# Optimization experiments

Measured on AMD Instinct MI355X. Metric: run time of the kernel, lower is better.

## Reference

```python
import jax, jax.numpy as jnp
import numpy as np

B, T, D, H, K, M = 2, 2048, 1024, 16, 3, 16384
HD = D // H
SCALE = D * (H ** 0.5)  # faithful to source: n_embd / n_head**(-0.5)


def _normalize(v, axis=-1, eps=1e-12):
    # torch F.normalize: v / max(||v||, eps)
    n = jnp.sqrt(jnp.sum(v * v, axis=axis, keepdims=True))
    return v / jnp.maximum(n, eps)


def setup_inputs() -> dict:
    key = jax.random.key(0)
    ks = jax.random.split(key, 12)
    s = 1.0 / np.sqrt(D)
    return {
        "x": jax.random.normal(ks[0], (B, T, D), jnp.float32),
        "Wq": jax.random.normal(ks[1], (D, D), jnp.float32) * s,
        "bq": jax.random.normal(ks[2], (D,), jnp.float32) * 0.01,
        "Wk": jax.random.normal(ks[3], (D, D), jnp.float32) * s,
        "bk": jax.random.normal(ks[4], (D,), jnp.float32) * 0.01,
        "Wv": jax.random.normal(ks[5], (D, D), jnp.float32) * s,
        "bv": jax.random.normal(ks[6], (D,), jnp.float32) * 0.01,
        "Wo": jax.random.normal(ks[7], (D, D), jnp.float32) * s,
        "bo": jax.random.normal(ks[8], (D,), jnp.float32) * 0.01,
        "gate_bias": jax.random.normal(ks[9], (H, 1, 1), jnp.float32),
        "mem_bank": jax.random.normal(ks[10], (B, M, 2, D), jnp.float32) * s,
        "knn_idx": jax.random.randint(ks[11], (B, T, K), 0, M, jnp.int32),
    }


def reference(x, Wq, bq, Wk, bk, Wv, bv, Wo, bo, gate_bias, mem_bank, knn_idx):
    b, t, d = x.shape
    # projections + L2-normalize q,k (as in source)
    q = _normalize(x @ Wq.T + bq)
    k = _normalize(x @ Wk.T + bk)
    v = x @ Wv.T + bv
    # split heads: b t (h hd) -> b h t hd
    q = q.reshape(b, t, H, HD).transpose(0, 2, 1, 3)
    k = k.reshape(b, t, H, HD).transpose(0, 2, 1, 3)
    v = v.reshape(b, t, H, HD).transpose(0, 2, 1, 3)
    # local causal attention (hand-rolled, dropout is eval no-op)
    qk = jnp.einsum('bhid,bhjd->bhij', q, k) * SCALE  # [b,h,t,t]
    causal = jnp.triu(jnp.ones((t, t), dtype=bool), 1)
    qk = jnp.where(causal, -jnp.inf, qk)
    attn = jax.nn.softmax(qk, axis=-1)
    qkv = jnp.einsum('bhij,bhjd->bhid', attn, v)  # [b,h,t,hd]
    # kNN memory retrieval: gather top-k (key,value) memories per token
    mem = mem_bank[jnp.arange(b)[:, None, None], knn_idx]  # [b,t,k,2,D]
    mem_k = mem[..., 0, :].reshape(b, t, K, H, HD).transpose(0, 3, 1, 2, 4)  # [b,h,t,k,hd]
    mem_v = mem[..., 1, :].reshape(b, t, K, H, HD).transpose(0, 3, 1, 2, 4)
    mem_qk = jnp.einsum('bhtd,bhtkd->bhtk', q.astype(jnp.float32), mem_k) * SCALE
    mem_attn = jax.nn.softmax(mem_qk, axis=-1)
    mem_qkv = jnp.einsum('bhtk,bhtkd->bhtd', mem_attn, mem_v)
    # per-head gated blend, bf16 round-trip (source casts to bfloat16)
    combined = mem_qkv * gate_bias + qkv * (1.0 - gate_bias)  # gate [H,1,1] broadcasts
    combined = combined.astype(jnp.bfloat16).astype(jnp.float32)
    y = combined.transpose(0, 2, 1, 3).reshape(b, t, d)  # b h t hd -> b t D
    return y @ Wo.T + bo
```

## Files before the change

kernel.cpp:

```cpp
#include <hip/hip_runtime.h>
#include <math.h>

#define B_ 2
#define T_ 2048
#define D_ 1024
#define H_ 16
#define HD_ 64
#define M_ 16384
#define SCALE_F 4096.0f
#define LDP 3072
#define ST 72

using short8 = __attribute__((ext_vector_type(8))) short;
using bf16x8 = __attribute__((ext_vector_type(8))) __bf16;
using f32x4  = __attribute__((ext_vector_type(4))) float;

__device__ __forceinline__ unsigned short f2bf(float x){
  unsigned u = __builtin_bit_cast(unsigned, x);
  u += 0x7fffu + ((u >> 16) & 1u);
  return (unsigned short)(u >> 16);
}
__device__ __forceinline__ float bf2f(unsigned short h){
  unsigned u = ((unsigned)h) << 16;
  return __builtin_bit_cast(float, u);
}

__device__ __forceinline__ float wsum(float v){
  #pragma unroll
  for (int off = 32; off; off >>= 1) v += __shfl_xor(v, off);
  return v;
}

__device__ __forceinline__ void ld_g2l16(const unsigned short* g, unsigned short* l){
  __builtin_amdgcn_global_load_lds(
      (const __attribute__((address_space(1))) void*)g,
      (__attribute__((address_space(3))) void*)l, 16, 0, 0);
}

__global__ __launch_bounds__(256)
void cvt_all(const float* __restrict__ x, const float* __restrict__ Wq,
             const float* __restrict__ Wk, const float* __restrict__ Wv,
             const float* __restrict__ Wo,
             unsigned short* __restrict__ Xhi, unsigned short* __restrict__ Xlo,
             unsigned short* __restrict__ Whi, unsigned short* __restrict__ Wlo,
             unsigned short* __restrict__ Wohi)
{
  const int i = blockIdx.x*256 + threadIdx.x;
  const float* src; unsigned short* hi; unsigned short* lo = nullptr; int rel;
  if      (i < 1048576){ src = x;  hi = Xhi;            lo = Xlo;            rel = i; }
  else if (i < 1310720){ src = Wq; hi = Whi;            lo = Wlo;            rel = i - 1048576; }
  else if (i < 1572864){ src = Wk; hi = Whi + 1048576;  lo = Wlo + 1048576;  rel = i - 1310720; }
  else if (i < 1835008){ src = Wv; hi = Whi + 2097152;                       rel = i - 1572864; }
  else                 { src = Wo; hi = Wohi;                                rel = i - 1835008; }
  float4 v = *(const float4*)(src + (size_t)rel*4);
  unsigned short h0=f2bf(v.x), h1=f2bf(v.y), h2=f2bf(v.z), h3=f2bf(v.w);
  uint2 hh; hh.x = (unsigned)h0 | ((unsigned)h1 << 16);
            hh.y = (unsigned)h2 | ((unsigned)h3 << 16);
  *(uint2*)(hi + (size_t)rel*4) = hh;
  if (lo){
    uint2 ll;
    ll.x = (unsigned)f2bf(v.x-bf2f(h0)) | ((unsigned)f2bf(v.y-bf2f(h1)) << 16);
    ll.y = (unsigned)f2bf(v.z-bf2f(h2)) | ((unsigned)f2bf(v.w-bf2f(h3)) << 16);
    *(uint2*)(lo + (size_t)rel*4) = ll;
  }
}

template<bool COMP>
__global__ __launch_bounds__(256)
void gemm_lds(const unsigned short* __restrict__ Ahi_g, const unsigned short* __restrict__ Alo_g,
              const unsigned short* __restrict__ Bhi_g, const unsigned short* __restrict__ Blo_g,
              const float* __restrict__ bias0, const float* __restrict__ bias1,
              const float* __restrict__ bias2,
              float* __restrict__ C, int ldc)
{
  __shared__ __align__(16) unsigned short Ah[128*32];
  __shared__ __align__(16) unsigned short Bh[128*32];
  __shared__ __align__(16) unsigned short Al[COMP ? 128*32 : 8];
  __shared__ __align__(16) unsigned short Bl[COMP ? 128*32 : 8];

  const int tid = threadIdx.x, lane = tid & 63, wv = tid >> 6;
  const int wm = wv >> 1, wn = wv & 1;
  const int mi = lane & 15, quad = lane >> 4;
  const int n0 = blockIdx.x * 128;
  const int m0 = blockIdx.y * 128;
  const int seg = n0 >> 10;
  const float* bias = (seg == 0) ? bias0 : (seg == 1) ? bias1 : bias2;
  const int nw = n0 & 1023;
  const bool comp = COMP && (seg < 2);

  f32x4 acc[4][4];
  #pragma unroll
  for (int a = 0; a < 4; ++a)
    #pragma unroll
    for (int b = 0; b < 4; ++b)
      acc[a][b] = (f32x4){0.f, 0.f, 0.f, 0.f};

  for (int k0 = 0; k0 < 1024; k0 += 32){
    __syncthreads();
    #pragma unroll
    for (int t = 0; t < 2; ++t){
      int j = wv*128 + t*64 + lane;
      int row = j >> 2, c16 = j & 3;
      size_t ga = (size_t)(m0 + row)*1024 + k0 + c16*8;
      size_t gb = (size_t)(n0 + row)*1024 + k0 + c16*8;
      ld_g2l16(Ahi_g + ga, Ah + j*8);
      ld_g2l16(Bhi_g + gb, Bh + j*8);
      if (comp){
        ld_g2l16(Alo_g + ga, Al + j*8);
        ld_g2l16(Blo_g + gb, Bl + j*8);
      }
    }
    __syncthreads();

    bf16x8 ah[4], al[4];
    #pragma unroll
    for (int a = 0; a < 4; ++a){
      int r = wm*64 + a*16 + mi;
      ah[a] = __builtin_bit_cast(bf16x8, *(const short8*)(Ah + r*32 + quad*8));
      if (comp)
        al[a] = __builtin_bit_cast(bf16x8, *(const short8*)(Al + r*32 + quad*8));
    }
    #pragma unroll
    for (int b = 0; b < 4; ++b){
      int r = wn*64 + b*16 + mi;
      bf16x8 bh = __builtin_bit_cast(bf16x8, *(const short8*)(Bh + r*32 + quad*8));
      if (comp){
        bf16x8 bl = __builtin_bit_cast(bf16x8, *(const short8*)(Bl + r*32 + quad*8));
        #pragma unroll
        for (int a = 0; a < 4; ++a){
          acc[a][b] = __builtin_amdgcn_mfma_f32_16x16x32_bf16(al[a], bh, acc[a][b], 0, 0, 0);
          acc[a][b] = __builtin_amdgcn_mfma_f32_16x16x32_bf16(ah[a], bl, acc[a][b], 0, 0, 0);
          acc[a][b] = __builtin_amdgcn_mfma_f32_16x16x32_bf16(ah[a], bh, acc[a][b], 0, 0, 0);
        }
      } else {
        #pragma unroll
        for (int a = 0; a < 4; ++a)
          acc[a][b] = __builtin_amdgcn_mfma_f32_16x16x32_bf16(ah[a], bh, acc[a][b], 0, 0, 0);
      }
    }
  }
  #pragma unroll
  for (int a = 0; a < 4; ++a)
    #pragma unroll
    for (int b = 0; b < 4; ++b)
      #pragma unroll
      for (int r = 0; r < 4; ++r){
        int row  = m0 + wm*64 + a*16 + quad*4 + r;
        int coll = wn*64 + b*16 + mi;
        C[(size_t)row*ldc + n0 + coll] = acc[a][b][r] + bias[nw + coll];
      }
}

__global__ __launch_bounds__(256)
void norm_split(const float* __restrict__ P,
                unsigned short* __restrict__ Qhi, unsigned short* __restrict__ Qlo,
                unsigned short* __restrict__ Khi, unsigned short* __restrict__ Klo,
                unsigned short* __restrict__ Vbf)
{
  const int row = blockIdx.x, tid = threadIdx.x;
  const int bb = row >> 11, t = row & 2047;
  const int lane = tid & 63, wv = tid >> 6;
  const size_t base = (size_t)row * LDP;
  float4 q4 = *(const float4*)(P + base + tid*4);
  float4 k4 = *(const float4*)(P + base + 1024 + tid*4);
  float4 v4 = *(const float4*)(P + base + 2048 + tid*4);
  float sq = wsum(q4.x*q4.x + q4.y*q4.y + q4.z*q4.z + q4.w*q4.w);
  float sk = wsum(k4.x*k4.x + k4.y*k4.y + k4.z*k4.z + k4.w*k4.w);
  __shared__ float rq[4], rk[4];
  if (lane == 0){ rq[wv] = sq; rk[wv] = sk; }
  __syncthreads();
  float cq = 1.f / fmaxf(sqrtf(rq[0]+rq[1]+rq[2]+rq[3]), 1e-12f);
  float ck = 1.f / fmaxf(sqrtf(rk[0]+rk[1]+rk[2]+rk[3]), 1e-12f);
  float qf[4] = {q4.x*cq, q4.y*cq, q4.z*cq, q4.w*cq};
  float kf[4] = {k4.x*ck, k4.y*ck, k4.z*ck, k4.w*ck};

  const int h = tid >> 4, d0 = (tid & 15)*4;
  const size_t ob = ((size_t)(bb*H_ + h)*T_ + t)*64 + d0;

  uint2 qh, ql, kh, kl, vv;
  unsigned short t0,t1,t2,t3;
  t0=f2bf(qf[0]); t1=f2bf(qf[1]); t2=f2bf(qf[2]); t3=f2bf(qf[3]);
  qh.x = t0 | ((unsigned)t1<<16); qh.y = t2 | ((unsigned)t3<<16);
  ql.x = f2bf(qf[0]-bf2f(t0)) | ((unsigned)f2bf(qf[1]-bf2f(t1))<<16);
  ql.y = f2bf(qf[2]-bf2f(t2)) | ((unsigned)f2bf(qf[3]-bf2f(t3))<<16);
  t0=f2bf(kf[0]); t1=f2bf(kf[1]); t2=f2bf(kf[2]); t3=f2bf(kf[3]);
  kh.x = t0 | ((unsigned)t1<<16); kh.y = t2 | ((unsigned)t3<<16);
  kl.x = f2bf(kf[0]-bf2f(t0)) | ((unsigned)f2bf(kf[1]-bf2f(t1))<<16);
  kl.y = f2bf(kf[2]-bf2f(t2)) | ((unsigned)f2bf(kf[3]-bf2f(t3))<<16);
  vv.x = f2bf(v4.x) | ((unsigned)f2bf(v4.y)<<16);
  vv.y = f2bf(v4.z) | ((unsigned)f2bf(v4.w)<<16);
  *(uint2*)(Qhi + ob) = qh;  *(uint2*)(Qlo + ob) = ql;
  *(uint2*)(Khi + ob) = kh;  *(uint2*)(Klo + ob) = kl;
  *(uint2*)(Vbf + ob) = vv;
}

__device__ __forceinline__ void attn_tile(
    const unsigned short* __restrict__ Kh, const unsigned short* __restrict__ Kl,
    const unsigned short* __restrict__ Vt, unsigned short* __restrict__ pw,
    const bf16x8* qh, const bf16x8* ql,
    f32x4* O, float& mr, float& lr,
    bool last, int relrow, int mi, int quad)
{
  f32x4 st[4];
  #pragma unroll
  for (int mt = 0; mt < 4; ++mt) st[mt] = (f32x4){0.f,0.f,0.f,0.f};
  #pragma unroll
  for (int mt = 0; mt < 4; ++mt){
    int krow = mt*16 + mi;
    #pragma unroll
    for (int ks = 0; ks < 2; ++ks){
      bf16x8 kh = __builtin_bit_cast(bf16x8, *(const short8*)(Kh + krow*ST + ks*32 + quad*8));
      bf16x8 kl = __builtin_bit_cast(bf16x8, *(const short8*)(Kl + krow*ST + ks*32 + quad*8));
      st[mt] = __builtin_amdgcn_mfma_f32_16x16x32_bf16(kl, qh[ks], st[mt], 0, 0, 0);
      st[mt] = __builtin_amdgcn_mfma_f32_16x16x32_bf16(kh, ql[ks], st[mt], 0, 0, 0);
      st[mt] = __builtin_amdgcn_mfma_f32_16x16x32_bf16(kh, qh[ks], st[mt], 0, 0, 0);
    }
  }

  float tmax = -INFINITY;
  #pragma unroll
  for (int mt = 0; mt < 4; ++mt)
    #pragma unroll
    for (int r = 0; r < 4; ++r){
      float s = st[mt][r] * SCALE_F;
      if (last){
        int key = mt*16 + quad*4 + r;
        if (key > relrow) s = -INFINITY;
      }
      st[mt][r] = s;
      tmax = fmaxf(tmax, s);
    }
  tmax = fmaxf(tmax, __shfl_xor(tmax, 16));
  tmax = fmaxf(tmax, __shfl_xor(tmax, 32));
  float mnew = fmaxf(mr, tmax);
  float alpha = __expf(mr - mnew);
  mr = mnew;
  float tsum = 0.f;
  #pragma unroll
  for (int mt = 0; mt < 4; ++mt)
    #pragma unroll
    for (int r = 0; r < 4; ++r){
      float p = __expf(st[mt][r] - mnew);
      st[mt][r] = p;
      tsum += p;
    }
  tsum += __shfl_xor(tsum, 16);
  tsum += __shfl_xor(tsum, 32);
  lr = lr*alpha + tsum;

  #pragma unroll
  for (int mt = 0; mt < 4; ++mt){
    uint2 pk;
    pk.x = (unsigned)f2bf(st[mt][0]) | ((unsigned)f2bf(st[mt][1]) << 16);
    pk.y = (unsigned)f2bf(st[mt][2]) | ((unsigned)f2bf(st[mt][3]) << 16);
    *(uint2*)(pw + mi*ST + mt*16 + quad*4) = pk;
  }

  float af[4];
  #pragma unroll
  for (int r = 0; r < 4; ++r) af[r] = __shfl(alpha, quad*4 + r);
  #pragma unroll
  for (int dn = 0; dn < 4; ++dn)
    #pragma unroll
    for (int r = 0; r < 4; ++r) O[dn][r] *= af[r];

  #pragma unroll
  for (int kt = 0; kt < 2; ++kt){
    bf16x8 pf = __builtin_bit_cast(bf16x8, *(const short8*)(pw + mi*ST + kt*32 + quad*8));
    #pragma unroll
    for (int dn = 0; dn < 4; ++dn){
      bf16x8 vf = __builtin_bit_cast(bf16x8, *(const short8*)(Vt + (dn*16 + mi)*ST + kt*32 + quad*8));
      O[dn] = __builtin_amdgcn_mfma_f32_16x16x32_bf16(pf, vf, O[dn], 0, 0, 0);
    }
  }
}

__global__ __launch_bounds__(256)
void attn_knn(const unsigned short* __restrict__ Qhi, const unsigned short* __restrict__ Qlo,
              const unsigned short* __restrict__ Khi_g, const unsigned short* __restrict__ Klo_g,
              const unsigned short* __restrict__ Vbf,
              const float* __restrict__ mem_bank, const int* __restrict__ knn_idx,
              const float* __restrict__ gate_bias, unsigned short* __restrict__ comb)
{
  __shared__ char smpool[36864];
  unsigned short* Kh = (unsigned short*)smpool;
  unsigned short* Kl = (unsigned short*)(smpool + 9216);
  unsigned short* Vt = (unsigned short*)(smpool + 18432);
  unsigned short* Pb = (unsigned short*)(smpool + 27648);
  float* qkvs = (float*)smpool;

  const int bb = blockIdx.z, h = blockIdx.y;
  const int p = blockIdx.x;
  const int jA = p, jB = 31 - p;
  const int tid = threadIdx.x, lane = tid & 63, wv = tid >> 6;
  const int mi = lane & 15, quad = lane >> 4;
  const int relrow = wv*16 + mi;
  const size_t hb = (size_t)(bb*H_ + h)*T_;
  unsigned short* pw = Pb + wv*1152;

  bf16x8 qhA[2], qlA[2], qhB[2], qlB[2];
  #pragma unroll
  for (int ks = 0; ks < 2; ++ks){
    qhA[ks] = __builtin_bit_cast(bf16x8, *(const uint4*)(Qhi + (hb + jA*64 + relrow)*64 + ks*32 + quad*8));
    qlA[ks] = __builtin_bit_cast(bf16x8, *(const uint4*)(Qlo + (hb + jA*64 + relrow)*64 + ks*32 + quad*8));
    qhB[ks] = __builtin_bit_cast(bf16x8, *(const uint4*)(Qhi + (hb + jB*64 + relrow)*64 + ks*32 + quad*8));
    qlB[ks] = __builtin_bit_cast(bf16x8, *(const uint4*)(Qlo + (hb + jB*64 + relrow)*64 + ks*32 + quad*8));
  }

  f32x4 OA[4], OB[4];
  #pragma unroll
  for (int dn = 0; dn < 4; ++dn){
    OA[dn] = (f32x4){0.f,0.f,0.f,0.f};
    OB[dn] = (f32x4){0.f,0.f,0.f,0.f};
  }
  float mA = -INFINITY, lA = 0.f, mB = -INFINITY, lB = 0.f;

  const int ntiles = jB + 1;
  for (int jt = 0; jt < ntiles; ++jt){
    __syncthreads();
    #pragma unroll
    for (int i = 0; i < 4; ++i){
      int idx = tid + i*256;
      int row = idx >> 4, c4 = idx & 15;
      size_t g = (hb + jt*64 + row)*64 + c4*4;
      *(uint2*)(Kh + row*ST + c4*4) = *(const uint2*)(Khi_g + g);
      *(uint2*)(Kl + row*ST + c4*4) = *(const uint2*)(Klo_g + g);
    }
    #pragma unroll
    for (int i = 0; i < 2; ++i){
      int idx = tid + i*256;
      int rp = idx & 31, d4 = idx >> 5;
      size_t g = (hb + jt*64 + 2*rp)*64 + d4*4;
      ushort4 a = *(const ushort4*)(Vbf + g);
      ushort4 b = *(const ushort4*)(Vbf + g + 64);
      unsigned* vt = (unsigned*)Vt;
      vt[(d4*4+0)*36 + rp] = (unsigned)a.x | ((unsigned)b.x << 16);
      vt[(d4*4+1)*36 + rp] = (unsigned)a.y | ((unsigned)b.y << 16);
      vt[(d4*4+2)*36 + rp] = (unsigned)a.z | ((unsigned)b.z << 16);
      vt[(d4*4+3)*36 + rp] = (unsigned)a.w | ((unsigned)b.w << 16);
    }
    __syncthreads();

    if (jt <= jA)
      attn_tile(Kh, Kl, Vt, pw, qhA, qlA, OA, mA, lA, jt == jA, relrow, mi, quad);
    attn_tile(Kh, Kl, Vt, pw, qhB, qlB, OB, mB, lB, jt == jB, relrow, mi, quad);
  }

  __syncthreads();
  {
    float liA[4], liB[4];
    #pragma unroll
    for (int r = 0; r < 4; ++r){
      liA[r] = 1.f / __shfl(lA, quad*4 + r);
      liB[r] = 1.f / __shfl(lB, quad*4 + r);
    }
    #pragma unroll
    for (int dn = 0; dn < 4; ++dn)
      #pragma unroll
      for (int r = 0; r < 4; ++r){
        qkvs[(      wv*16 + quad*4 + r)*68 + dn*16 + mi] = OA[dn][r] * liA[r];
        qkvs[(64 +  wv*16 + quad*4 + r)*68 + dn*16 + mi] = OB[dn][r] * liB[r];
      }
  }
  __syncthreads();

  const float g = gate_bias[h];
  const float gq = 1.f - g;
  const int sub = lane & 3;
  const int grp = tid >> 2;
  const int base = lane & 60;

  #pragma unroll
  for (int it = 0; it < 2; ++it){
    const int jq = it ? jB : jA;
    const int trow = jq*64 + grp;
    const int lrow = it*64 + grp;
    const int* kidx = knn_idx + ((size_t)bb*T_ + trow)*3;
    int myidx = 0;
    if (sub < 3) myidx = kidx[sub];

    float qf[16];
    {
      const unsigned short* qp = Qhi + (hb + trow)*64 + sub*16;
      const unsigned short* lp = Qlo + (hb + trow)*64 + sub*16;
      unsigned short hs[16], ls[16];
      *(uint4*)hs     = *(const uint4*)qp;
      *(uint4*)(hs+8) = *(const uint4*)(qp+8);
      *(uint4*)ls     = *(const uint4*)lp;
      *(uint4*)(ls+8) = *(const uint4*)(lp+8);
      #pragma unroll
      for (int j = 0; j < 16; ++j) qf[j] = bf2f(hs[j]) + bf2f(ls[j]);
    }

    int idxs[3]; float dts[3]; float mx = -INFINITY;
    #pragma unroll
    for (int kk = 0; kk < 3; ++kk){
      int idx = __shfl(myidx, base + kk);
      idxs[kk] = idx;
      const float* mk = mem_bank + (((size_t)bb*M_ + idx)*2 + 0)*D_ + h*HD_ + sub*16;
      float dsum = 0.f;
      #pragma unroll
      for (int j4 = 0; j4 < 4; ++j4){
        float4 m4 = *(const float4*)(mk + j4*4);
        dsum += qf[j4*4+0]*m4.x + qf[j4*4+1]*m4.y + qf[j4*4+2]*m4.z + qf[j4*4+3]*m4.w;
      }
      dsum += __shfl_xor(dsum, 1);
      dsum += __shfl_xor(dsum, 2);
      dsum *= SCALE_F;
      dts[kk] = dsum;
      mx = fmaxf(mx, dsum);
    }
    float e0 = __expf(dts[0]-mx), e1 = __expf(dts[1]-mx), e2 = __expf(dts[2]-mx);
    float inv = 1.f/(e0+e1+e2);
    float w[3] = {e0*inv, e1*inv, e2*inv};

    float ov[16];
    #pragma unroll
    for (int j = 0; j < 16; ++j) ov[j] = 0.f;
    #pragma unroll
    for (int kk = 0; kk < 3; ++kk){
      const float* mv = mem_bank + (((size_t)bb*M_ + idxs[kk])*2 + 1)*D_ + h*HD_ + sub*16;
      #pragma unroll
      for (int j4 = 0; j4 < 4; ++j4){
        float4 m4 = *(const float4*)(mv + j4*4);
        ov[j4*4+0] += w[kk]*m4.x;
        ov[j4*4+1] += w[kk]*m4.y;
        ov[j4*4+2] += w[kk]*m4.z;
        ov[j4*4+3] += w[kk]*m4.w;
      }
    }

    unsigned short os[16];
    #pragma unroll
    for (int j = 0; j < 16; ++j){
      float qkv = qkvs[lrow*68 + sub*16 + j];
      os[j] = f2bf(ov[j]*g + qkv*gq);
    }
    unsigned short* op = comb + ((size_t)bb*T_ + trow)*D_ + h*HD_ + sub*16;
    *(uint4*)op     = *(uint4*)os;
    *(uint4*)(op+8) = *(uint4*)(os+8);
  }
}

extern "C" void kernel_launch(void* const* d_in, const int* in_sizes, int n_in,
                              void* d_out, int out_size, void* d_ws, size_t ws_size,
                              hipStream_t stream)
{
  (void)in_sizes; (void)n_in; (void)out_size; (void)ws_size;
  const float* x    = (const float*)d_in[0];
  const float* Wq   = (const float*)d_in[1];
  const float* bq   = (const float*)d_in[2];
  const float* Wk   = (const float*)d_in[3];
  const float* bk   = (const float*)d_in[4];
  const float* Wv   = (const float*)d_in[5];
  const float* bv   = (const float*)d_in[6];
  const float* Wo   = (const float*)d_in[7];
  const float* bo   = (const float*)d_in[8];
  const float* gate = (const float*)d_in[9];
  const float* mem  = (const float*)d_in[10];
  const int*   knn  = (const int*)d_in[11];

  char* ws = (char*)d_ws;
  float*          P    = (float*)ws;
  unsigned short* comb = (unsigned short*)ws;
  unsigned short* Qhi  = (unsigned short*)(ws +  50331648);
  unsigned short* Qlo  = (unsigned short*)(ws +  58720256);
  unsigned short* Khi  = (unsigned short*)(ws +  67108864);
  unsigned short* Klo  = (unsigned short*)(ws +  75497472);
  unsigned short* Vbf  = (unsigned short*)(ws +  83886080);
  unsigned short* Xhi  = (unsigned short*)(ws +  92274688);
  unsigned short* Xlo  = (unsigned short*)(ws + 100663296);
  unsigned short* Whi  = (unsigned short*)(ws + 109051904);
  unsigned short* Wlo  = (unsigned short*)(ws + 115343360);
  unsigned short* Wohi = (unsigned short*)(ws + 119537664);

  cvt_all<<<8192, 256, 0, stream>>>(x, Wq, Wk, Wv, Wo, Xhi, Xlo, Whi, Wlo, Wohi);
  gemm_lds<true><<<dim3(24, 32), 256, 0, stream>>>(Xhi, Xlo, Whi, Wlo, bq, bk, bv, P, LDP);
  norm_split<<<4096, 256, 0, stream>>>(P, Qhi, Qlo, Khi, Klo, Vbf);
  attn_knn<<<dim3(T_/128, H_, B_), 256, 0, stream>>>(Qhi, Qlo, Khi, Klo, Vbf,
                                                     mem, knn, gate, comb);
  gemm_lds<false><<<dim3(8, 32), 256, 0, stream>>>(comb, nullptr, Wohi, nullptr,
                                                   bo, bo, bo, (float*)d_out, D_);
}
```

Baseline: 586.0 us.

## Double-buffer K/V tiles in attention with register prefetch, add MFMA priority and GEMM block swizzle

The attention kernel now keeps two LDS buffers for K/V tiles and prefetches the tile after next into registers, so global loads overlap the MFMA work on the current tile and one barrier per iteration is removed. MFMA sections are wrapped in s_setprio to favour matrix issue. The GEMM remaps block IDs in an XCD-aware interleave (groups of 8) for better L2 locality. LDS use grows from about 36KB to 63KB per block, which may reduce occupancy, and holding the prefetch registers raises register pressure.

```diff
diff --git a/kernel.cpp b/kernel.cpp
--- a/kernel.cpp
+++ b/kernel.cpp
@@ -81,8 +81,13 @@
   const int tid = threadIdx.x, lane = tid & 63, wv = tid >> 6;
   const int wm = wv >> 1, wn = wv & 1;
   const int mi = lane & 15, quad = lane >> 4;
-  const int n0 = blockIdx.x * 128;
-  const int m0 = blockIdx.y * 128;
+
+  int bid = blockIdx.y*gridDim.x + blockIdx.x;
+  const int cpx = (gridDim.x*gridDim.y) >> 3;
+  bid = (bid & 7)*cpx + (bid >> 3);
+  const int n0 = (bid % gridDim.x) * 128;
+  const int m0 = (bid / gridDim.x) * 128;
+
   const int seg = n0 >> 10;
   const float* bias = (seg == 0) ? bias0 : (seg == 1) ? bias1 : bias2;
   const int nw = n0 & 1023;
@@ -194,6 +199,53 @@
   *(uint2*)(Vbf + ob) = vv;
 }
 
+__device__ __forceinline__ void stage_issue(
+    const unsigned short* __restrict__ Khi_g, const unsigned short* __restrict__ Klo_g,
+    const unsigned short* __restrict__ Vbf, size_t hb, int jt, int tid,
+    uint2* khr, uint2* klr, ushort4* vra, ushort4* vrb)
+{
+  #pragma unroll
+  for (int i = 0; i < 4; ++i){
+    int idx = tid + i*256;
+    int row = idx >> 4, c4 = idx & 15;
+    size_t g = (hb + jt*64 + row)*64 + c4*4;
+    khr[i] = *(const uint2*)(Khi_g + g);
+    klr[i] = *(const uint2*)(Klo_g + g);
+  }
+  #pragma unroll
+  for (int i = 0; i < 2; ++i){
+    int idx = tid + i*256;
+    int rp = idx & 31, d4 = idx >> 5;
+    size_t g = (hb + jt*64 + 2*rp)*64 + d4*4;
+    vra[i] = *(const ushort4*)(Vbf + g);
+    vrb[i] = *(const ushort4*)(Vbf + g + 64);
+  }
+}
+
+__device__ __forceinline__ void stage_write(char* bufc, int tid,
+    const uint2* khr, const uint2* klr, const ushort4* vra, const ushort4* vrb)
+{
+  unsigned short* Kh = (unsigned short*)bufc;
+  unsigned short* Kl = (unsigned short*)(bufc + 9216);
+  unsigned* vt = (unsigned*)(bufc + 18432);
+  #pragma unroll
+  for (int i = 0; i < 4; ++i){
+    int idx = tid + i*256;
+    int row = idx >> 4, c4 = idx & 15;
+    *(uint2*)(Kh + row*ST + c4*4) = khr[i];
+    *(uint2*)(Kl + row*ST + c4*4) = klr[i];
+  }
+  #pragma unroll
+  for (int i = 0; i < 2; ++i){
+    int idx = tid + i*256;
+    int rp = idx & 31, d4 = idx >> 5;
+    vt[(d4*4+0)*36 + rp] = (unsigned)vra[i].x | ((unsigned)vrb[i].x << 16);
+    vt[(d4*4+1)*36 + rp] = (unsigned)vra[i].y | ((unsigned)vrb[i].y << 16);
+    vt[(d4*4+2)*36 + rp] = (unsigned)vra[i].z | ((unsigned)vrb[i].z << 16);
+    vt[(d4*4+3)*36 + rp] = (unsigned)vra[i].w | ((unsigned)vrb[i].w << 16);
+  }
+}
+
 __device__ __forceinline__ void attn_tile(
     const unsigned short* __restrict__ Kh, const unsigned short* __restrict__ Kl,
     const unsigned short* __restrict__ Vt, unsigned short* __restrict__ pw,
@@ -204,6 +256,7 @@
   f32x4 st[4];
   #pragma unroll
   for (int mt = 0; mt < 4; ++mt) st[mt] = (f32x4){0.f,0.f,0.f,0.f};
+  __builtin_amdgcn_s_setprio(1);
   #pragma unroll
   for (int mt = 0; mt < 4; ++mt){
     int krow = mt*16 + mi;
@@ -216,6 +269,7 @@
       st[mt] = __builtin_amdgcn_mfma_f32_16x16x32_bf16(kh, qh[ks], st[mt], 0, 0, 0);
     }
   }
+  __builtin_amdgcn_s_setprio(0);
 
   float tmax = -INFINITY;
   #pragma unroll
@@ -264,6 +318,7 @@
     #pragma unroll
     for (int r = 0; r < 4; ++r) O[dn][r] *= af[r];
 
+  __builtin_amdgcn_s_setprio(1);
   #pragma unroll
   for (int kt = 0; kt < 2; ++kt){
     bf16x8 pf = __builtin_bit_cast(bf16x8, *(const short8*)(pw + mi*ST + kt*32 + quad*8));
@@ -273,6 +328,7 @@
       O[dn] = __builtin_amdgcn_mfma_f32_16x16x32_bf16(pf, vf, O[dn], 0, 0, 0);
     }
   }
+  __builtin_amdgcn_s_setprio(0);
 }
 
 __global__ __launch_bounds__(256)
@@ -282,11 +338,7 @@
               const float* __restrict__ mem_bank, const int* __restrict__ knn_idx,
               const float* __restrict__ gate_bias, unsigned short* __restrict__ comb)
 {
-  __shared__ char smpool[36864];
-  unsigned short* Kh = (unsigned short*)smpool;
-  unsigned short* Kl = (unsigned short*)(smpool + 9216);
-  unsigned short* Vt = (unsigned short*)(smpool + 18432);
-  unsigned short* Pb = (unsigned short*)(smpool + 27648);
+  __shared__ __align__(16) char smpool[64512];
   float* qkvs = (float*)smpool;
 
   const int bb = blockIdx.z, h = blockIdx.y;
@@ -296,7 +348,7 @@
   const int mi = lane & 15, quad = lane >> 4;
   const int relrow = wv*16 + mi;
   const size_t hb = (size_t)(bb*H_ + h)*T_;
-  unsigned short* pw = Pb + wv*1152;
+  unsigned short* pw = (unsigned short*)(smpool + 55296) + wv*1152;
 
   bf16x8 qhA[2], qlA[2], qhB[2], qlB[2];
   #pragma unroll
@@ -316,34 +368,28 @@
   float mA = -INFINITY, lA = 0.f, mB = -INFINITY, lB = 0.f;
 
   const int ntiles = jB + 1;
+
+  uint2 khr[4], klr[4]; ushort4 vra[2], vrb[2];
+  stage_issue(Khi_g, Klo_g, Vbf, hb, 0, tid, khr, klr, vra, vrb);
+  stage_write(smpool, tid, khr, klr, vra, vrb);
+  stage_issue(Khi_g, Klo_g, Vbf, hb, 1, tid, khr, klr, vra, vrb);
+
+  int cur = 0;
   for (int jt = 0; jt < ntiles; ++jt){
     __syncthreads();
-    #pragma unroll
-    for (int i = 0; i < 4; ++i){
-      int idx = tid + i*256;
-      int row = idx >> 4, c4 = idx & 15;
-      size_t g = (hb + jt*64 + row)*64 + c4*4;
-      *(uint2*)(Kh + row*ST + c4*4) = *(const uint2*)(Khi_g + g);
-      *(uint2*)(Kl + row*ST + c4*4) = *(const uint2*)(Klo_g + g);
-    }
-    #pragma unroll
-    for (int i = 0; i < 2; ++i){
-      int idx = tid + i*256;
-      int rp = idx & 31, d4 = idx >> 5;
-      size_t g = (hb + jt*64 + 2*rp)*64 + d4*4;
-      ushort4 a = *(const ushort4*)(Vbf + g);
-      ushort4 b = *(const ushort4*)(Vbf + g + 64);
-      unsigned* vt = (unsigned*)Vt;
-      vt[(d4*4+0)*36 + rp] = (unsigned)a.x | ((unsigned)b.x << 16);
-      vt[(d4*4+1)*36 + rp] = (unsigned)a.y | ((unsigned)b.y << 16);
-      vt[(d4*4+2)*36 + rp] = (unsigned)a.z | ((unsigned)b.z << 16);
-      vt[(d4*4+3)*36 + rp] = (unsigned)a.w | ((unsigned)b.w << 16);
-    }
-    __syncthreads();
-
+    if (jt + 1 < ntiles){
+      stage_write(smpool + (cur^1)*27648, tid, khr, klr, vra, vrb);
+      if (jt + 2 < ntiles)
+        stage_issue(Khi_g, Klo_g, Vbf, hb, jt+2, tid, khr, klr, vra, vrb);
+    }
+    char* bufc = smpool + cur*27648;
+    const unsigned short* Kh = (const unsigned short*)bufc;
+    const unsigned short* Kl = (const unsigned short*)(bufc + 9216);
+    const unsigned short* Vt = (const unsigned short*)(bufc + 18432);
     if (jt <= jA)
       attn_tile(Kh, Kl, Vt, pw, qhA, qlA, OA, mA, lA, jt == jA, relrow, mi, quad);
     attn_tile(Kh, Kl, Vt, pw, qhB, qlB, OB, mB, lB, jt == jB, relrow, mi, quad);
+    cur ^= 1;
   }
 
   __syncthreads();
```

Measured after the change: 557.0 us. 5.0% less time.
